# Kernel optimization log

Measured on AMD Instinct MI355X. Metric: run time of the kernel, lower is better.

The kernel has to match this reference:

```python
import jax, jax.numpy as jnp
from jax import lax
import numpy as np

GAMMA = 0.1      # sinkhorn_alpha
EPS = 0.005      # stop_thr
MAXITERS = 1000  # OT_max_iter
TINY = 1e-30


def _pairwise_sq_dist(x, y):
    return (jnp.sum(x * x, axis=1, keepdims=True)
            + jnp.sum(y * y, axis=1)[None, :]
            - 2.0 * (x @ y.T))


def _sinkhorn(M, r, c):
    # M: (B,H,W); r: (1,H); c: (1,W). Faithful to _sinkhorn_inline.
    r_ = r[:, :, None]          # (1,H,1)
    c_ = c[:, None, :]          # (1,W,1 -> 1,1,W)
    M_min = jnp.min(M, axis=2, keepdims=True)
    P0 = jnp.exp(-GAMMA * (M - M_min))

    def cond(state):
        _, err, it = state
        return (err > EPS) & (it < MAXITERS)

    def body(state):
        P, _, it = state
        alpha = jnp.sum(P, axis=2, keepdims=True)
        P1 = P / jnp.maximum(alpha, TINY) * r_
        beta = jnp.sum(P1, axis=1, keepdims=True)
        err = jnp.max(jnp.sum(jnp.abs(beta - c_), axis=2))
        P2 = P1 / jnp.maximum(beta, TINY) * c_
        # torch breaks BEFORE the column update when converged -> keep P1 then
        Pn = jnp.where(err <= EPS, P1, P2)
        return Pn, err, it + 1

    init = (P0, jnp.asarray(jnp.inf, M.dtype), jnp.asarray(0, jnp.int32))
    P, _, _ = lax.while_loop(cond, body, init)
    return P


def setup_inputs() -> dict:
    key = jax.random.key(0)
    k1, k2 = jax.random.split(key)
    x = jax.random.normal(k1, (1024, 512), dtype=jnp.float32)
    y = jax.random.normal(k2, (16384, 512), dtype=jnp.float32)
    return {"x": x, "y": y}


def reference(x, y):
    M = _pairwise_sq_dist(x, y)           # (n, m)
    n, m = M.shape
    # init_a_dist / init_b_dist are None -> uniform marginals (already normalized)
    a = jnp.full((1, n), 1.0 / n, dtype=M.dtype)
    b = jnp.full((1, m), 1.0 / m, dtype=M.dtype)
    # n <= m by construction -> implicit path takes the non-transpose branch
    P = _sinkhorn(M[None], a, b)[0]       # (n, m)
    loss_ETP = jnp.sum(P * M)
    return loss_ETP, P
```

## Files before the change

### kernel.cpp

```cpp
#include <hip/hip_runtime.h>

#define N_ROWS 1024
#define M_COLS 16384
#define DIM 512

constexpr float GAMMA_ = 0.1f;
constexpr float INV_GAMMA = 10.0f;
constexpr float EPS_ = 0.005f;
constexpr float TINY_ = 1e-30f;
constexpr float RVAL = 1.0f / 1024.0f;
constexpr float CVAL = 1.0f / 16384.0f;

typedef __attribute__((ext_vector_type(8))) short bf16x8;
typedef __attribute__((ext_vector_type(4))) float f32x4;

__device__ __forceinline__ float waveRedSum(float v) {
#pragma unroll
    for (int o = 32; o > 0; o >>= 1) v += __shfl_down(v, o);
    return v;
}
__device__ __forceinline__ float waveRedMin(float v) {
#pragma unroll
    for (int o = 32; o > 0; o >>= 1) v = fminf(v, __shfl_down(v, o));
    return v;
}

__device__ __forceinline__ unsigned sysloadu(const unsigned* p) {
    return __hip_atomic_load(p, __ATOMIC_RELAXED, __HIP_MEMORY_SCOPE_SYSTEM);
}
__device__ __forceinline__ void sysstoreu(unsigned* p, unsigned v) {
    __hip_atomic_store(p, v, __ATOMIC_RELAXED, __HIP_MEMORY_SCOPE_SYSTEM);
}
__device__ __forceinline__ float sysloadf(const float* p) {
    return __hip_atomic_load(p, __ATOMIC_RELAXED, __HIP_MEMORY_SCOPE_SYSTEM);
}
__device__ __forceinline__ void sysstoref(float* p, float v) {
    __hip_atomic_store(p, v, __ATOMIC_RELAXED, __HIP_MEMORY_SCOPE_SYSTEM);
}

__device__ __forceinline__ void gbarx(unsigned* __restrict__ arr, unsigned* __restrict__ bcast,
                                      int b, int tid, unsigned e) {
    __syncthreads();
    if (tid == 0) sysstoreu(&arr[b], e);
    if (b == 0) {
        if (tid < 256) {
            while (sysloadu(&arr[tid]) < e) __builtin_amdgcn_s_sleep(1);
        }
        __syncthreads();
        if (tid == 0) sysstoreu(bcast, e);
    } else {
        if (tid == 0) {
            while (sysloadu(bcast) < e) __builtin_amdgcn_s_sleep(1);
        }
    }
    __syncthreads();
}

__device__ __forceinline__ unsigned bf16b(float f) {
    unsigned u = __float_as_uint(f);
    return (u + 0x7FFFu + ((u >> 16) & 1u)) >> 16;
}

__global__ void conv_x(const float* __restrict__ X, unsigned short* __restrict__ xh,
                       unsigned short* __restrict__ xl, float* __restrict__ sx) {
    const int row = blockIdx.x, t = threadIdx.x;
    const float* xr = X + (size_t)row * DIM + t * 8;
    float4 a = *(const float4*)xr, c = *(const float4*)(xr + 4);
    float v[8] = {a.x, a.y, a.z, a.w, c.x, c.y, c.z, c.w};
    unsigned hs[8], ls[8];
    float sq = 0.f;
#pragma unroll
    for (int j = 0; j < 8; ++j) {
        unsigned h = bf16b(v[j]);
        hs[j] = h;
        ls[j] = bf16b(v[j] - __uint_as_float(h << 16));
        sq = fmaf(v[j], v[j], sq);
    }
    uint4 hv = make_uint4(hs[0] | (hs[1] << 16), hs[2] | (hs[3] << 16),
                          hs[4] | (hs[5] << 16), hs[6] | (hs[7] << 16));
    uint4 lv = make_uint4(ls[0] | (ls[1] << 16), ls[2] | (ls[3] << 16),
                          ls[4] | (ls[5] << 16), ls[6] | (ls[7] << 16));
    const size_t off = (size_t)row * 1024 + t * 16;
    *(uint4*)((char*)xh + off) = hv;
    *(uint4*)((char*)xl + off) = lv;
    sq = waveRedSum(sq);
    if (t == 0) sx[row] = sq;
}

__global__ void conv_y(const float* __restrict__ Y, unsigned short* __restrict__ yh,
                       unsigned short* __restrict__ yl, float* __restrict__ sy) {
    const int row = blockIdx.x, t = threadIdx.x;
    const float* yr = Y + (size_t)row * DIM + t * 8;
    float4 a = *(const float4*)yr, c = *(const float4*)(yr + 4);
    float v[8] = {a.x, a.y, a.z, a.w, c.x, c.y, c.z, c.w};
    unsigned hs[8], ls[8];
    float sq = 0.f;
#pragma unroll
    for (int j = 0; j < 8; ++j) {
        unsigned h = bf16b(v[j]);
        hs[j] = h;
        ls[j] = bf16b(v[j] - __uint_as_float(h << 16));
        sq = fmaf(v[j], v[j], sq);
    }
    uint4 hv = make_uint4(hs[0] | (hs[1] << 16), hs[2] | (hs[3] << 16),
                          hs[4] | (hs[5] << 16), hs[6] | (hs[7] << 16));
    uint4 lv = make_uint4(ls[0] | (ls[1] << 16), ls[2] | (ls[3] << 16),
                          ls[4] | (ls[5] << 16), ls[6] | (ls[7] << 16));
    const size_t off = ((size_t)row * 1024 + t * 16) ^ ((size_t)((row & 7) << 4));
    *(uint4*)((char*)yh + off) = hv;
    *(uint4*)((char*)yl + off) = lv;
    sq = waveRedSum(sq);
    if (t == 0) sy[row] = sq;
}

__global__ void init_state(float* __restrict__ ubuf, unsigned* __restrict__ bar,
                           float* __restrict__ out) {
    int idx = blockIdx.x * blockDim.x + threadIdx.x;
    if (idx < 512) bar[idx] = 0u;
    if (idx < 1024) { ubuf[idx] = 1.0f; ubuf[1024 + idx] = 1.0f; }
    if (idx == 0) out[0] = 0.0f;
}

__global__ __launch_bounds__(1024, 4) void sinkhorn_full(
        const unsigned short* __restrict__ xh, const unsigned short* __restrict__ xl,
        const unsigned short* __restrict__ yh, const unsigned short* __restrict__ yl,
        const float* __restrict__ sx, const float* __restrict__ sy,
        float* __restrict__ ubuf, float* __restrict__ Mming,
        float* __restrict__ out, unsigned* __restrict__ bar) {
    const int tid = threadIdx.x;
    const int b = blockIdx.x;
    const int lane = tid & 63;
    const int w = tid >> 6;
    const int l15 = lane & 15;
    const int q = lane >> 4;
    float* Pbuf = out + 1;
    float* spart = out + 4;
    float* errpart = out + 270000;
    unsigned* arr = bar;
    unsigned* bcast = bar + 288;

    __shared__ __align__(16) char ldsY[131072];
    __shared__ float sx_lds[1024];
    __shared__ float mmin_lds[1024];
    __shared__ float u_lds[1024];
    __shared__ float sy_lds[64];
    __shared__ float v_lds[2][64];
    __shared__ float t_acc[16][68];
    __shared__ float red[16];
    __shared__ float sh_err;

    {
        const char* ysrcH = (const char*)yh + (size_t)b * 65536;
        const char* ysrcL = (const char*)yl + (size_t)b * 65536;
#pragma unroll
        for (int p = 0; p < 4; ++p) {
            const int d = tid * 16 + p * 16384;
            *(uint4*)(ldsY + d) = *(const uint4*)(ysrcH + d);
            *(uint4*)(ldsY + 65536 + d) = *(const uint4*)(ysrcL + d);
        }
        sx_lds[tid] = sx[tid];
        if (tid < 64) {
            sy_lds[tid] = sy[(b << 6) + tid];
            v_lds[0][tid] = 1.0f;
            v_lds[1][tid] = 1.0f;
        }
    }
    __syncthreads();

    f32x4 kf[4][4] = {};
    {
        const int rowbase = (w << 6) + l15;
        const int kofs = q * 8;
#pragma unroll 1
        for (int ks = 0; ks < 16; ++ks) {
            bf16x8 ah[4], al[4], bh[4], bl[4];
#pragma unroll
            for (int i = 0; i < 4; ++i) {
                const size_t xo = (size_t)(rowbase + i * 16) * 512 + ks * 32 + kofs;
                ah[i] = *(const bf16x8*)(xh + xo);
                al[i] = *(const bf16x8*)(xl + xo);
                const int cl = i * 16 + l15;
                const int bo = (cl * 1024 + ks * 64 + q * 16) ^ ((cl & 7) << 4);
                bh[i] = *(const bf16x8*)(ldsY + bo);
                bl[i] = *(const bf16x8*)(ldsY + 65536 + bo);
            }
#pragma unroll
            for (int i = 0; i < 4; ++i)
#pragma unroll
                for (int j = 0; j < 4; ++j) {
                    kf[i][j] = __builtin_amdgcn_mfma_f32_16x16x32_bf16(ah[i], bh[j], kf[i][j], 0, 0, 0);
                    kf[i][j] = __builtin_amdgcn_mfma_f32_16x16x32_bf16(ah[i], bl[j], kf[i][j], 0, 0, 0);
                    kf[i][j] = __builtin_amdgcn_mfma_f32_16x16x32_bf16(al[i], bh[j], kf[i][j], 0, 0, 0);
                }
        }
    }
#pragma unroll
    for (int i = 0; i < 4; ++i)
#pragma unroll
        for (int j = 0; j < 4; ++j) {
            const float syv = sy_lds[j * 16 + l15];
#pragma unroll
            for (int reg = 0; reg < 4; ++reg) {
                const int r = (w << 6) + i * 16 + (q << 2) + reg;
                kf[i][j][reg] = sx_lds[r] + syv - 2.0f * kf[i][j][reg];
            }
        }
    {
        float mn[4][4];
#pragma unroll
        for (int i = 0; i < 4; ++i)
#pragma unroll
            for (int reg = 0; reg < 4; ++reg) {
                float m = fminf(fminf(kf[i][0][reg], kf[i][1][reg]),
                                fminf(kf[i][2][reg], kf[i][3][reg]));
#pragma unroll
                for (int o = 1; o < 16; o <<= 1) m = fminf(m, __shfl_xor(m, o));
                mn[i][reg] = m;
            }
        if (l15 == 0) {
#pragma unroll
            for (int i = 0; i < 4; ++i)
#pragma unroll
                for (int reg = 0; reg < 4; ++reg) {
                    const int r = (w << 6) + i * 16 + (q << 2) + reg;
                    sysstoref(&spart[(size_t)r * 256 + b], mn[i][reg]);
                }
        }
    }
    gbarx(arr, bcast, b, tid, 1u);
    if (w >= 1 && w <= 4) {
        const int r = (b << 2) + (w - 1);
        const float* sp = spart + (size_t)r * 256;
        float m = fminf(fminf(sysloadf(&sp[lane]), sysloadf(&sp[lane + 64])),
                        fminf(sysloadf(&sp[lane + 128]), sysloadf(&sp[lane + 192])));
        m = waveRedMin(m);
        if (lane == 0) sysstoref(&Mming[r], m);
    }
    gbarx(arr, bcast, b, tid, 2u);
    if (tid < 256) {
#pragma unroll
        for (int k2 = 0; k2 < 4; ++k2) mmin_lds[tid * 4 + k2] = sysloadf(&Mming[tid * 4 + k2]);
    }
    __syncthreads();
#pragma unroll
    for (int i = 0; i < 4; ++i)
#pragma unroll
        for (int j = 0; j < 4; ++j)
#pragma unroll
            for (int reg = 0; reg < 4; ++reg) {
                const int r = (w << 6) + i * 16 + (q << 2) + reg;
                kf[i][j][reg] = __expf(-GAMMA_ * (kf[i][j][reg] - mmin_lds[r]));
            }

    int cur = 0, vsel = 0, brk = 0;
    unsigned ep = 3u;
    int it = 0;
    for (;; ++it, ep += 2u) {
        {
            float vv[4];
#pragma unroll
            for (int j = 0; j < 4; ++j) vv[j] = v_lds[cur][j * 16 + l15];
            float rs[4][4];
#pragma unroll
            for (int i = 0; i < 4; ++i)
#pragma unroll
                for (int reg = 0; reg < 4; ++reg) {
                    float p = kf[i][0][reg] * vv[0];
                    p = fmaf(kf[i][1][reg], vv[1], p);
                    p = fmaf(kf[i][2][reg], vv[2], p);
                    p = fmaf(kf[i][3][reg], vv[3], p);
#pragma unroll
                    for (int o = 1; o < 16; o <<= 1) p += __shfl_xor(p, o);
                    rs[i][reg] = p;
                }
            if (l15 == 0) {
#pragma unroll
                for (int i = 0; i < 4; ++i)
#pragma unroll
                    for (int reg = 0; reg < 4; ++reg) {
                        const int r = (w << 6) + i * 16 + (q << 2) + reg;
                        sysstoref(&spart[(size_t)r * 256 + b], rs[i][reg]);
                    }
            }
        }
        gbarx(arr, bcast, b, tid, ep);
        float* uOld = ubuf + (((it & 1) ^ 1) << 10);
        float* uNew = ubuf + ((it & 1) << 10);
        {
            if (w == 0) {
                float e = 0.f;
                if (it > 0)
                    e = sysloadf(&errpart[lane]) + sysloadf(&errpart[lane + 64]) +
                        sysloadf(&errpart[lane + 128]) + sysloadf(&errpart[lane + 192]);
                e = waveRedSum(e);
                if (lane == 0) sh_err = (it > 0) ? e : 1e30f;
            } else if (w <= 4) {
                const int r = (b << 2) + (w - 1);
                const float* sp = spart + (size_t)r * 256;
                float s = sysloadf(&sp[lane]) + sysloadf(&sp[lane + 64]) +
                          sysloadf(&sp[lane + 128]) + sysloadf(&sp[lane + 192]);
                s = waveRedSum(s);
                if (lane == 0) {
                    float uo = sysloadf(&uOld[r]);
                    sysstoref(&uNew[r], uo * RVAL / fmaxf(uo * s, TINY_));
                }
            }
        }
        __syncthreads();
        float err = sh_err;
        brk = (err <= EPS_) ? 1 : ((it == 1000) ? 2 : 0);
        gbarx(arr, bcast, b, tid, ep + 1u);
        if (brk) { vsel = (brk == 1) ? (cur ^ 1) : cur; break; }
        if (tid < 256) {
#pragma unroll
            for (int k2 = 0; k2 < 4; ++k2) u_lds[tid * 4 + k2] = sysloadf(&uNew[tid * 4 + k2]);
        }
        __syncthreads();
        {
            float uu[4][4];
#pragma unroll
            for (int i = 0; i < 4; ++i)
#pragma unroll
                for (int reg = 0; reg < 4; ++reg)
                    uu[i][reg] = u_lds[(w << 6) + i * 16 + (q << 2) + reg];
            float tj[4];
#pragma unroll
            for (int j = 0; j < 4; ++j) {
                float t = 0.f;
#pragma unroll
                for (int i = 0; i < 4; ++i)
#pragma unroll
                    for (int reg = 0; reg < 4; ++reg)
                        t = fmaf(kf[i][j][reg], uu[i][reg], t);
                t += __shfl_xor(t, 16);
                t += __shfl_xor(t, 32);
                tj[j] = t;
            }
            if (q == 0) {
#pragma unroll
                for (int j = 0; j < 4; ++j) t_acc[w][j * 16 + l15] = tj[j];
            }
        }
        __syncthreads();
        if (tid < 64) {
            float t = 0.f;
#pragma unroll
            for (int w2 = 0; w2 < 16; ++w2) t += t_acc[w2][tid];
            float vc = v_lds[cur][tid];
            float beta = vc * t;
            float e = fabsf(beta - CVAL);
            v_lds[cur ^ 1][tid] = vc * CVAL / fmaxf(beta, TINY_);
            e = waveRedSum(e);
            if (tid == 0) sysstoref(&errpart[b], e);
        }
        __syncthreads();
        cur ^= 1;
    }

    const float* uEpi = ubuf + (((it & 1) ^ 1) << 10);
    if (tid < 256) {
#pragma unroll
        for (int k2 = 0; k2 < 4; ++k2) u_lds[tid * 4 + k2] = sysloadf(&uEpi[tid * 4 + k2]);
    }
    __syncthreads();
    float vv[4];
#pragma unroll
    for (int j = 0; j < 4; ++j) vv[j] = v_lds[vsel][j * 16 + l15];
    float lsum = 0.f;
#pragma unroll
    for (int i = 0; i < 4; ++i)
#pragma unroll
        for (int reg = 0; reg < 4; ++reg) {
            const int r = (w << 6) + i * 16 + (q << 2) + reg;
            const float ur = u_lds[r];
            const float mmr = mmin_lds[r];
            float* prow = Pbuf + (size_t)r * M_COLS + (b << 6) + l15;
#pragma unroll
            for (int j = 0; j < 4; ++j) {
                float kv = kf[i][j][reg];
                float p = 0.f;
                if (kv > 0.f) {
                    p = ur * kv * vv[j];
                    lsum = fmaf(p, mmr - __logf(kv) * INV_GAMMA, lsum);
                }
                prow[j * 16] = p;
            }
        }
    lsum = waveRedSum(lsum);
    if (lane == 0) red[w] = lsum;
    __syncthreads();
    if (tid == 0) {
        float s = 0.f;
#pragma unroll
        for (int i2 = 0; i2 < 16; ++i2) s += red[i2];
        atomicAdd(out, s);
    }
}

extern "C" void kernel_launch(void* const* d_in, const int* in_sizes, int n_in,
                              void* d_out, int out_size, void* d_ws, size_t ws_size,
                              hipStream_t stream) {
    const float* x = (const float*)d_in[0];
    const float* y = (const float*)d_in[1];
    float* out = (float*)d_out;
    float* ws = (float*)d_ws;
    float* sx   = ws;
    float* sy   = ws + 1024;
    float* Mming = ws + 17408;
    float* ubuf = ws + 18432;
    unsigned* bar = (unsigned*)(ws + 20480);

    unsigned short* xh = (unsigned short*)(out + 300000);
    unsigned short* xl = (unsigned short*)(out + 600000);
    unsigned short* yh = (unsigned short*)(out + 900000);
    unsigned short* yl = (unsigned short*)(out + 5200000);

    conv_x<<<N_ROWS, 64, 0, stream>>>(x, xh, xl, sx);
    conv_y<<<M_COLS, 64, 0, stream>>>(y, yh, yl, sy);
    init_state<<<4, 256, 0, stream>>>(ubuf, bar, out);
    {
        const unsigned short *xhc = xh, *xlc = xl, *yhc = yh, *ylc = yl;
        const float *sxc = sx, *syc = sy;
        void* args[] = {(void*)&xhc, (void*)&xlc, (void*)&yhc, (void*)&ylc,
                        (void*)&sxc, (void*)&syc, (void*)&ubuf, (void*)&Mming,
                        (void*)&out, (void*)&bar};
        hipLaunchCooperativeKernel((const void*)sinkhorn_full, dim3(256), dim3(1024), args, 0, stream);
    }
}
```

Measured before the change: 235.8 us.

## Replace two-barrier-per-iteration grid sync with a hierarchical per-XCD tree exchange

Swaps the centralized global barrier, and the extra reduction phase that followed it, for a two-level tree exchange. Blocks are grouped by XCD (b&7), eight leader blocks reduce their group's partials, and every block then combines the eight group results itself. Every block now computes the full u vector redundantly in LDS instead of going through a global u buffer, and the column error is carried along with the next iteration's row partials. This cuts the global barriers per Sinkhorn iteration from two to one and removes the u broadcast round trip, at the cost of more redundant reads by each block and larger scratch buffers placed far into the output region.

```diff
diff --git a/kernel.cpp b/kernel.cpp
--- a/kernel.cpp
+++ b/kernel.cpp
@@ -19,11 +19,6 @@
     for (int o = 32; o > 0; o >>= 1) v += __shfl_down(v, o);
     return v;
 }
-__device__ __forceinline__ float waveRedMin(float v) {
-#pragma unroll
-    for (int o = 32; o > 0; o >>= 1) v = fminf(v, __shfl_down(v, o));
-    return v;
-}
 
 __device__ __forceinline__ unsigned sysloadu(const unsigned* p) {
     return __hip_atomic_load(p, __ATOMIC_RELAXED, __HIP_MEMORY_SCOPE_SYSTEM);
@@ -36,29 +31,61 @@
 }
 __device__ __forceinline__ void sysstoref(float* p, float v) {
     __hip_atomic_store(p, v, __ATOMIC_RELAXED, __HIP_MEMORY_SCOPE_SYSTEM);
-}
-
-__device__ __forceinline__ void gbarx(unsigned* __restrict__ arr, unsigned* __restrict__ bcast,
-                                      int b, int tid, unsigned e) {
-    __syncthreads();
-    if (tid == 0) sysstoreu(&arr[b], e);
-    if (b == 0) {
-        if (tid < 256) {
-            while (sysloadu(&arr[tid]) < e) __builtin_amdgcn_s_sleep(1);
-        }
-        __syncthreads();
-        if (tid == 0) sysstoreu(bcast, e);
-    } else {
-        if (tid == 0) {
-            while (sysloadu(bcast) < e) __builtin_amdgcn_s_sleep(1);
-        }
-    }
-    __syncthreads();
 }
 
 __device__ __forceinline__ unsigned bf16b(float f) {
     unsigned u = __float_as_uint(f);
     return (u + 0x7FFFu + ((u >> 16) & 1u)) >> 16;
+}
+
+template<bool MINOP>
+__device__ __forceinline__ float tree_exchange(float* __restrict__ spart2,
+        float* __restrict__ sxcd, unsigned* __restrict__ warr,
+        unsigned* __restrict__ xcdrep, const int b, const int tid,
+        const int p, const unsigned ep, const bool doErr) {
+    const int g = b & 7, w32 = b >> 3;
+    __syncthreads();
+    if (tid == 0) sysstoreu(&warr[(g << 5) + w32], ep);
+    if (b < 8) {
+        if (tid < 32) {
+            while (sysloadu(&warr[(b << 5) + tid]) < ep) __builtin_amdgcn_s_sleep(1);
+        }
+        __syncthreads();
+        {
+            const float* sp = spart2 + ((size_t)((p << 3) + b) * 1056 + tid) * 32;
+            float tv[32];
+#pragma unroll
+            for (int i = 0; i < 32; ++i) tv[i] = sysloadf(&sp[i]);
+            float v0 = tv[0];
+#pragma unroll
+            for (int i = 1; i < 32; ++i) v0 = MINOP ? fminf(v0, tv[i]) : (v0 + tv[i]);
+            sysstoref(&sxcd[((size_t)p * 1025 + tid) * 8 + b], v0);
+            if (!MINOP && doErr && tid == 0) {
+                const float* epr = spart2 + ((size_t)((p << 3) + b) * 1056 + 1024) * 32;
+                float ev[32];
+#pragma unroll
+                for (int i = 0; i < 32; ++i) ev[i] = sysloadf(&epr[i]);
+                float es = ev[0];
+#pragma unroll
+                for (int i = 1; i < 32; ++i) es += ev[i];
+                sysstoref(&sxcd[((size_t)p * 1025 + 1024) * 8 + b], es);
+            }
+        }
+        __syncthreads();
+        if (tid < 32) sysstoreu(&xcdrep[(b << 5) + tid], ep);
+    }
+    if (tid < 8) {
+        while (sysloadu(&xcdrep[(tid << 5) + w32]) < ep) __builtin_amdgcn_s_sleep(1);
+    }
+    __syncthreads();
+    const float* sr = sxcd + ((size_t)p * 1025 + tid) * 8;
+    float rv[8];
+#pragma unroll
+    for (int i = 0; i < 8; ++i) rv[i] = sysloadf(&sr[i]);
+    float r = rv[0];
+#pragma unroll
+    for (int i = 1; i < 8; ++i) r = MINOP ? fminf(r, rv[i]) : (r + rv[i]);
+    return r;
 }
 
 __global__ void conv_x(const float* __restrict__ X, unsigned short* __restrict__ xh,
@@ -113,41 +140,40 @@
     if (t == 0) sy[row] = sq;
 }
 
-__global__ void init_state(float* __restrict__ ubuf, unsigned* __restrict__ bar,
-                           float* __restrict__ out) {
+__global__ void init_state(unsigned* __restrict__ flags, float* __restrict__ out) {
     int idx = blockIdx.x * blockDim.x + threadIdx.x;
-    if (idx < 512) bar[idx] = 0u;
-    if (idx < 1024) { ubuf[idx] = 1.0f; ubuf[1024 + idx] = 1.0f; }
+    if (idx < 512) flags[idx] = 0u;
     if (idx == 0) out[0] = 0.0f;
 }
 
-__global__ __launch_bounds__(1024, 4) void sinkhorn_full(
+__global__ __launch_bounds__(1024) void sinkhorn_full(
         const unsigned short* __restrict__ xh, const unsigned short* __restrict__ xl,
         const unsigned short* __restrict__ yh, const unsigned short* __restrict__ yl,
         const float* __restrict__ sx, const float* __restrict__ sy,
-        float* __restrict__ ubuf, float* __restrict__ Mming,
-        float* __restrict__ out, unsigned* __restrict__ bar) {
+        float* __restrict__ sxcd, unsigned* __restrict__ flags,
+        float* __restrict__ out) {
     const int tid = threadIdx.x;
     const int b = blockIdx.x;
     const int lane = tid & 63;
     const int w = tid >> 6;
     const int l15 = lane & 15;
     const int q = lane >> 4;
+    const int g = b & 7, w32 = b >> 3;
     float* Pbuf = out + 1;
-    float* spart = out + 4;
-    float* errpart = out + 270000;
-    unsigned* arr = bar;
-    unsigned* bcast = bar + 288;
+    float* spart2 = out + 10000000;
+    unsigned* warr = flags;
+    unsigned* xcdrep = flags + 256;
 
     __shared__ __align__(16) char ldsY[131072];
     __shared__ float sx_lds[1024];
     __shared__ float mmin_lds[1024];
-    __shared__ float u_lds[1024];
+    __shared__ float u_lds[2][1024];
     __shared__ float sy_lds[64];
     __shared__ float v_lds[2][64];
     __shared__ float t_acc[16][68];
     __shared__ float red[16];
     __shared__ float sh_err;
+    __shared__ float sh_eprev;
 
     {
         const char* ysrcH = (const char*)yh + (size_t)b * 65536;
@@ -159,11 +185,14 @@
             *(uint4*)(ldsY + 65536 + d) = *(const uint4*)(ysrcL + d);
         }
         sx_lds[tid] = sx[tid];
+        u_lds[0][tid] = 1.0f;
+        u_lds[1][tid] = 1.0f;
         if (tid < 64) {
             sy_lds[tid] = sy[(b << 6) + tid];
             v_lds[0][tid] = 1.0f;
             v_lds[1][tid] = 1.0f;
         }
+        if (tid == 0) { sh_eprev = 0.0f; }
     }
     __syncthreads();
 
@@ -223,24 +252,11 @@
 #pragma unroll
                 for (int reg = 0; reg < 4; ++reg) {
                     const int r = (w << 6) + i * 16 + (q << 2) + reg;
-                    sysstoref(&spart[(size_t)r * 256 + b], mn[i][reg]);
+                    sysstoref(&spart2[((size_t)g * 1056 + r) * 32 + w32], mn[i][reg]);
                 }
         }
     }
-    gbarx(arr, bcast, b, tid, 1u);
-    if (w >= 1 && w <= 4) {
-        const int r = (b << 2) + (w - 1);
-        const float* sp = spart + (size_t)r * 256;
-        float m = fminf(fminf(sysloadf(&sp[lane]), sysloadf(&sp[lane + 64])),
-                        fminf(sysloadf(&sp[lane + 128]), sysloadf(&sp[lane + 192])));
-        m = waveRedMin(m);
-        if (lane == 0) sysstoref(&Mming[r], m);
-    }
-    gbarx(arr, bcast, b, tid, 2u);
-    if (tid < 256) {
-#pragma unroll
-        for (int k2 = 0; k2 < 4; ++k2) mmin_lds[tid * 4 + k2] = sysloadf(&Mming[tid * 4 + k2]);
-    }
+    mmin_lds[tid] = tree_exchange<true>(spart2, sxcd, warr, xcdrep, b, tid, 0, 1u, false);
     __syncthreads();
 #pragma unroll
     for (int i = 0; i < 4; ++i)
@@ -253,9 +269,10 @@
             }
 
     int cur = 0, vsel = 0, brk = 0;
-    unsigned ep = 3u;
     int it = 0;
-    for (;; ++it, ep += 2u) {
+    for (;; ++it) {
+        const int p = it & 1;
+        const unsigned ep = (unsigned)it + 2u;
         {
             float vv[4];
 #pragma unroll
@@ -265,13 +282,13 @@
             for (int i = 0; i < 4; ++i)
 #pragma unroll
                 for (int reg = 0; reg < 4; ++reg) {
-                    float p = kf[i][0][reg] * vv[0];
-                    p = fmaf(kf[i][1][reg], vv[1], p);
-                    p = fmaf(kf[i][2][reg], vv[2], p);
-                    p = fmaf(kf[i][3][reg], vv[3], p);
-#pragma unroll
-                    for (int o = 1; o < 16; o <<= 1) p += __shfl_xor(p, o);
-                    rs[i][reg] = p;
+                    float pp = kf[i][0][reg] * vv[0];
+                    pp = fmaf(kf[i][1][reg], vv[1], pp);
+                    pp = fmaf(kf[i][2][reg], vv[2], pp);
+                    pp = fmaf(kf[i][3][reg], vv[3], pp);
+#pragma unroll
+                    for (int o = 1; o < 16; o <<= 1) pp += __shfl_xor(pp, o);
+                    rs[i][reg] = pp;
                 }
             if (l15 == 0) {
 #pragma unroll
@@ -279,50 +296,40 @@
 #pragma unroll
                     for (int reg = 0; reg < 4; ++reg) {
                         const int r = (w << 6) + i * 16 + (q << 2) + reg;
-                        sysstoref(&spart[(size_t)r * 256 + b], rs[i][reg]);
+                        sysstoref(&spart2[((size_t)((p << 3) + g) * 1056 + r) * 32 + w32], rs[i][reg]);
                     }
             }
-        }
-        gbarx(arr, bcast, b, tid, ep);
-        float* uOld = ubuf + (((it & 1) ^ 1) << 10);
-        float* uNew = ubuf + ((it & 1) << 10);
+            if (tid == 0)
+                sysstoref(&spart2[((size_t)((p << 3) + g) * 1056 + 1024) * 32 + w32], sh_eprev);
+        }
+        float srow = tree_exchange<false>(spart2, sxcd, warr, xcdrep, b, tid, p, ep, true);
         {
-            if (w == 0) {
-                float e = 0.f;
-                if (it > 0)
-                    e = sysloadf(&errpart[lane]) + sysloadf(&errpart[lane + 64]) +
-                        sysloadf(&errpart[lane + 128]) + sysloadf(&errpart[lane + 192]);
-                e = waveRedSum(e);
-                if (lane == 0) sh_err = (it > 0) ? e : 1e30f;
-            } else if (w <= 4) {
-                const int r = (b << 2) + (w - 1);
-                const float* sp = spart + (size_t)r * 256;
-                float s = sysloadf(&sp[lane]) + sysloadf(&sp[lane + 64]) +
-                          sysloadf(&sp[lane + 128]) + sysloadf(&sp[lane + 192]);
-                s = waveRedSum(s);
-                if (lane == 0) {
-                    float uo = sysloadf(&uOld[r]);
-                    sysstoref(&uNew[r], uo * RVAL / fmaxf(uo * s, TINY_));
-                }
-            }
+            float uo = u_lds[p ^ 1][tid];
+            u_lds[p][tid] = uo * RVAL / fmaxf(uo * srow, TINY_);
+        }
+        if (tid == 0) {
+            float e = 0.f;
+            if (it > 0) {
+                const float* er = sxcd + ((size_t)p * 1025 + 1024) * 8;
+                float ev[8];
+#pragma unroll
+                for (int i = 0; i < 8; ++i) ev[i] = sysloadf(&er[i]);
+#pragma unroll
+                for (int i = 0; i < 8; ++i) e += ev[i];
+            }
+            sh_err = (it > 0) ? e : 1e30f;
         }
         __syncthreads();
         float err = sh_err;
         brk = (err <= EPS_) ? 1 : ((it == 1000) ? 2 : 0);
-        gbarx(arr, bcast, b, tid, ep + 1u);
         if (brk) { vsel = (brk == 1) ? (cur ^ 1) : cur; break; }
-        if (tid < 256) {
-#pragma unroll
-            for (int k2 = 0; k2 < 4; ++k2) u_lds[tid * 4 + k2] = sysloadf(&uNew[tid * 4 + k2]);
-        }
-        __syncthreads();
         {
             float uu[4][4];
 #pragma unroll
             for (int i = 0; i < 4; ++i)
 #pragma unroll
                 for (int reg = 0; reg < 4; ++reg)
-                    uu[i][reg] = u_lds[(w << 6) + i * 16 + (q << 2) + reg];
+                    uu[i][reg] = u_lds[p][(w << 6) + i * 16 + (q << 2) + reg];
             float tj[4];
 #pragma unroll
             for (int j = 0; j < 4; ++j) {
@@ -351,18 +358,13 @@
             float e = fabsf(beta - CVAL);
             v_lds[cur ^ 1][tid] = vc * CVAL / fmaxf(beta, TINY_);
             e = waveRedSum(e);
-            if (tid == 0) sysstoref(&errpart[b], e);
+            if (tid == 0) sh_eprev = e;
         }
         __syncthreads();
         cur ^= 1;
     }
 
-    const float* uEpi = ubuf + (((it & 1) ^ 1) << 10);
-    if (tid < 256) {
-#pragma unroll
-        for (int k2 = 0; k2 < 4; ++k2) u_lds[tid * 4 + k2] = sysloadf(&uEpi[tid * 4 + k2]);
-    }
-    __syncthreads();
+    const int usel = (it & 1) ^ 1;
     float vv[4];
 #pragma unroll
     for (int j = 0; j < 4; ++j) vv[j] = v_lds[vsel][j * 16 + l15];
@@ -372,18 +374,18 @@
 #pragma unroll
         for (int reg = 0; reg < 4; ++reg) {
             const int r = (w << 6) + i * 16 + (q << 2) + reg;
-            const float ur = u_lds[r];
+            const float ur = u_lds[usel][r];
             const float mmr = mmin_lds[r];
             float* prow = Pbuf + (size_t)r * M_COLS + (b << 6) + l15;
 #pragma unroll
             for (int j = 0; j < 4; ++j) {
                 float kv = kf[i][j][reg];
-                float p = 0.f;
+                float pv = 0.f;
                 if (kv > 0.f) {
-                    p = ur * kv * vv[j];
-                    lsum = fmaf(p, mmr - __logf(kv) * INV_GAMMA, lsum);
+                    pv = ur * kv * vv[j];
+                    lsum = fmaf(pv, mmr - __logf(kv) * INV_GAMMA, lsum);
                 }
-                prow[j * 16] = p;
+                prow[j * 16] = pv;
             }
         }
     lsum = waveRedSum(lsum);
@@ -406,9 +408,8 @@
     float* ws = (float*)d_ws;
     float* sx   = ws;
     float* sy   = ws + 1024;
-    float* Mming = ws + 17408;
-    float* ubuf = ws + 18432;
-    unsigned* bar = (unsigned*)(ws + 20480);
+    float* sxcd = ws + 18432;
+    unsigned* flags = (unsigned*)(ws + 36864);
 
     unsigned short* xh = (unsigned short*)(out + 300000);
     unsigned short* xl = (unsigned short*)(out + 600000);
@@ -417,13 +418,13 @@
 
     conv_x<<<N_ROWS, 64, 0, stream>>>(x, xh, xl, sx);
     conv_y<<<M_COLS, 64, 0, stream>>>(y, yh, yl, sy);
-    init_state<<<4, 256, 0, stream>>>(ubuf, bar, out);
+    init_state<<<2, 256, 0, stream>>>(flags, out);
     {
         const unsigned short *xhc = xh, *xlc = xl, *yhc = yh, *ylc = yl;
         const float *sxc = sx, *syc = sy;
         void* args[] = {(void*)&xhc, (void*)&xlc, (void*)&yhc, (void*)&ylc,
-                        (void*)&sxc, (void*)&syc, (void*)&ubuf, (void*)&Mming,
-                        (void*)&out, (void*)&bar};
+                        (void*)&sxc, (void*)&syc, (void*)&sxcd, (void*)&flags,
+                        (void*)&out};
         hipLaunchCooperativeKernel((const void*)sinkhorn_full, dim3(256), dim3(1024), args, 0, stream);
     }
 }
```

Result: slower. 355.8 us (+50.9%).

## Fuse Y bf16 split into Sinkhorn kernel and coalesce partial-sum exchange

Applied to the files above, without the earlier changes.

Removes the separate conv_y kernel. Each block now loads its 64 Y rows straight from fp32, splits them into bf16 hi/lo parts in LDS and computes the row squared norms locally. The global exchange of per-row partial sums is restructured: each block stages its 1024 values in LDS and writes them contiguously. The per-block error value is also piggybacked into the same buffer, which removes a separate errpart store per iteration. The cost is an extra __syncthreads per iteration and strided cross-block reads on the reduction side.

```diff
diff --git a/kernel.cpp b/kernel.cpp
--- a/kernel.cpp
+++ b/kernel.cpp
@@ -87,46 +87,20 @@
     if (t == 0) sx[row] = sq;
 }
 
-__global__ void conv_y(const float* __restrict__ Y, unsigned short* __restrict__ yh,
-                       unsigned short* __restrict__ yl, float* __restrict__ sy) {
-    const int row = blockIdx.x, t = threadIdx.x;
-    const float* yr = Y + (size_t)row * DIM + t * 8;
-    float4 a = *(const float4*)yr, c = *(const float4*)(yr + 4);
-    float v[8] = {a.x, a.y, a.z, a.w, c.x, c.y, c.z, c.w};
-    unsigned hs[8], ls[8];
-    float sq = 0.f;
-#pragma unroll
-    for (int j = 0; j < 8; ++j) {
-        unsigned h = bf16b(v[j]);
-        hs[j] = h;
-        ls[j] = bf16b(v[j] - __uint_as_float(h << 16));
-        sq = fmaf(v[j], v[j], sq);
-    }
-    uint4 hv = make_uint4(hs[0] | (hs[1] << 16), hs[2] | (hs[3] << 16),
-                          hs[4] | (hs[5] << 16), hs[6] | (hs[7] << 16));
-    uint4 lv = make_uint4(ls[0] | (ls[1] << 16), ls[2] | (ls[3] << 16),
-                          ls[4] | (ls[5] << 16), ls[6] | (ls[7] << 16));
-    const size_t off = ((size_t)row * 1024 + t * 16) ^ ((size_t)((row & 7) << 4));
-    *(uint4*)((char*)yh + off) = hv;
-    *(uint4*)((char*)yl + off) = lv;
-    sq = waveRedSum(sq);
-    if (t == 0) sy[row] = sq;
-}
-
-__global__ void init_state(float* __restrict__ ubuf, unsigned* __restrict__ bar,
+__global__ void init_state(float* __restrict__ ubuf, unsigned* __restrict__ flags,
                            float* __restrict__ out) {
     int idx = blockIdx.x * blockDim.x + threadIdx.x;
-    if (idx < 512) bar[idx] = 0u;
-    if (idx < 1024) { ubuf[idx] = 1.0f; ubuf[1024 + idx] = 1.0f; }
+    if (idx < 512) flags[idx] = 0u;
+    if (idx < 512) { ubuf[idx * 4] = 1.0f; ubuf[idx * 4 + 1] = 1.0f;
+                     ubuf[idx * 4 + 2] = 1.0f; ubuf[idx * 4 + 3] = 1.0f; }
     if (idx == 0) out[0] = 0.0f;
 }
 
 __global__ __launch_bounds__(1024, 4) void sinkhorn_full(
         const unsigned short* __restrict__ xh, const unsigned short* __restrict__ xl,
-        const unsigned short* __restrict__ yh, const unsigned short* __restrict__ yl,
-        const float* __restrict__ sx, const float* __restrict__ sy,
+        const float* __restrict__ Y, const float* __restrict__ sx,
         float* __restrict__ ubuf, float* __restrict__ Mming,
-        float* __restrict__ out, unsigned* __restrict__ bar) {
+        float* __restrict__ out, unsigned* __restrict__ flags) {
     const int tid = threadIdx.x;
     const int b = blockIdx.x;
     const int lane = tid & 63;
@@ -134,10 +108,9 @@
     const int l15 = lane & 15;
     const int q = lane >> 4;
     float* Pbuf = out + 1;
-    float* spart = out + 4;
-    float* errpart = out + 270000;
-    unsigned* arr = bar;
-    unsigned* bcast = bar + 288;
+    float* spart2 = out + 10000000;
+    unsigned* arr = flags;
+    unsigned* bcast = flags + 288;
 
     __shared__ __align__(16) char ldsY[131072];
     __shared__ float sx_lds[1024];
@@ -146,24 +119,48 @@
     __shared__ float sy_lds[64];
     __shared__ float v_lds[2][64];
     __shared__ float t_acc[16][68];
+    __shared__ float srow_lds[16][64];
     __shared__ float red[16];
     __shared__ float sh_err;
+    __shared__ float sh_eprev;
 
     {
-        const char* ysrcH = (const char*)yh + (size_t)b * 65536;
-        const char* ysrcL = (const char*)yl + (size_t)b * 65536;
-#pragma unroll
-        for (int p = 0; p < 4; ++p) {
-            const int d = tid * 16 + p * 16384;
-            *(uint4*)(ldsY + d) = *(const uint4*)(ysrcH + d);
-            *(uint4*)(ldsY + 65536 + d) = *(const uint4*)(ysrcL + d);
-        }
+        const int row = tid >> 4;
+        const int c = tid & 15;
+        const float* yr = Y + (size_t)((b << 6) + row) * DIM + c * 32;
+        const int swz = (row & 7) << 4;
+        float sq = 0.f;
+#pragma unroll
+        for (int s2 = 0; s2 < 4; ++s2) {
+            float4 f0 = *(const float4*)(yr + s2 * 8);
+            float4 f1 = *(const float4*)(yr + s2 * 8 + 4);
+            float v8[8] = {f0.x, f0.y, f0.z, f0.w, f1.x, f1.y, f1.z, f1.w};
+            unsigned h[8], lo[8];
+#pragma unroll
+            for (int j = 0; j < 8; ++j) {
+                h[j] = bf16b(v8[j]);
+                lo[j] = bf16b(v8[j] - __uint_as_float(h[j] << 16));
+                sq = fmaf(v8[j], v8[j], sq);
+            }
+            const int off = (row * 1024 + c * 64 + s2 * 16) ^ swz;
+            *(uint4*)(ldsY + off) = make_uint4(h[0] | (h[1] << 16), h[2] | (h[3] << 16),
+                                               h[4] | (h[5] << 16), h[6] | (h[7] << 16));
+            *(uint4*)(ldsY + 65536 + off) = make_uint4(lo[0] | (lo[1] << 16), lo[2] | (lo[3] << 16),
+                                                       lo[4] | (lo[5] << 16), lo[6] | (lo[7] << 16));
+        }
+        float* sy_part = (float*)t_acc;
+        sy_part[row * 17 + c] = sq;
         sx_lds[tid] = sx[tid];
-        if (tid < 64) {
-            sy_lds[tid] = sy[(b << 6) + tid];
-            v_lds[0][tid] = 1.0f;
-            v_lds[1][tid] = 1.0f;
-        }
+        if (tid < 64) { v_lds[0][tid] = 1.0f; v_lds[1][tid] = 1.0f; }
+        if (tid == 0) sh_eprev = 0.0f;
+    }
+    __syncthreads();
+    if (tid < 64) {
+        const float* sy_part = (const float*)t_acc;
+        float s = 0.f;
+#pragma unroll
+        for (int c2 = 0; c2 < 16; ++c2) s += sy_part[tid * 17 + c2];
+        sy_lds[tid] = s;
     }
     __syncthreads();
 
@@ -221,18 +218,19 @@
 #pragma unroll
             for (int i = 0; i < 4; ++i)
 #pragma unroll
-                for (int reg = 0; reg < 4; ++reg) {
-                    const int r = (w << 6) + i * 16 + (q << 2) + reg;
-                    sysstoref(&spart[(size_t)r * 256 + b], mn[i][reg]);
-                }
-        }
+                for (int reg = 0; reg < 4; ++reg)
+                    srow_lds[w][i * 16 + (q << 2) + reg] = mn[i][reg];
+        }
+        __syncthreads();
+        sysstoref(&spart2[(size_t)b * 1056 + (w << 6) + lane], srow_lds[w][lane]);
     }
     gbarx(arr, bcast, b, tid, 1u);
     if (w >= 1 && w <= 4) {
         const int r = (b << 2) + (w - 1);
-        const float* sp = spart + (size_t)r * 256;
-        float m = fminf(fminf(sysloadf(&sp[lane]), sysloadf(&sp[lane + 64])),
-                        fminf(sysloadf(&sp[lane + 128]), sysloadf(&sp[lane + 192])));
+        float m = fminf(fminf(sysloadf(&spart2[(size_t)lane * 1056 + r]),
+                              sysloadf(&spart2[(size_t)(lane + 64) * 1056 + r])),
+                        fminf(sysloadf(&spart2[(size_t)(lane + 128) * 1056 + r]),
+                              sysloadf(&spart2[(size_t)(lane + 192) * 1056 + r])));
         m = waveRedMin(m);
         if (lane == 0) sysstoref(&Mming[r], m);
     }
@@ -253,9 +251,9 @@
             }
 
     int cur = 0, vsel = 0, brk = 0;
-    unsigned ep = 3u;
     int it = 0;
-    for (;; ++it, ep += 2u) {
+    for (;; ++it) {
+        const unsigned ep = 3u + 2u * (unsigned)it;
         {
             float vv[4];
 #pragma unroll
@@ -265,23 +263,24 @@
             for (int i = 0; i < 4; ++i)
 #pragma unroll
                 for (int reg = 0; reg < 4; ++reg) {
-                    float p = kf[i][0][reg] * vv[0];
-                    p = fmaf(kf[i][1][reg], vv[1], p);
-                    p = fmaf(kf[i][2][reg], vv[2], p);
-                    p = fmaf(kf[i][3][reg], vv[3], p);
-#pragma unroll
-                    for (int o = 1; o < 16; o <<= 1) p += __shfl_xor(p, o);
-                    rs[i][reg] = p;
+                    float pp = kf[i][0][reg] * vv[0];
+                    pp = fmaf(kf[i][1][reg], vv[1], pp);
+                    pp = fmaf(kf[i][2][reg], vv[2], pp);
+                    pp = fmaf(kf[i][3][reg], vv[3], pp);
+#pragma unroll
+                    for (int o = 1; o < 16; o <<= 1) pp += __shfl_xor(pp, o);
+                    rs[i][reg] = pp;
                 }
             if (l15 == 0) {
 #pragma unroll
                 for (int i = 0; i < 4; ++i)
 #pragma unroll
-                    for (int reg = 0; reg < 4; ++reg) {
-                        const int r = (w << 6) + i * 16 + (q << 2) + reg;
-                        sysstoref(&spart[(size_t)r * 256 + b], rs[i][reg]);
-                    }
-            }
+                    for (int reg = 0; reg < 4; ++reg)
+                        srow_lds[w][i * 16 + (q << 2) + reg] = rs[i][reg];
+            }
+            __syncthreads();
+            sysstoref(&spart2[(size_t)b * 1056 + (w << 6) + lane], srow_lds[w][lane]);
+            if (tid == 0) sysstoref(&spart2[(size_t)b * 1056 + 1024], sh_eprev);
         }
         gbarx(arr, bcast, b, tid, ep);
         float* uOld = ubuf + (((it & 1) ^ 1) << 10);
@@ -290,15 +289,18 @@
             if (w == 0) {
                 float e = 0.f;
                 if (it > 0)
-                    e = sysloadf(&errpart[lane]) + sysloadf(&errpart[lane + 64]) +
-                        sysloadf(&errpart[lane + 128]) + sysloadf(&errpart[lane + 192]);
+                    e = sysloadf(&spart2[(size_t)lane * 1056 + 1024]) +
+                        sysloadf(&spart2[(size_t)(lane + 64) * 1056 + 1024]) +
+                        sysloadf(&spart2[(size_t)(lane + 128) * 1056 + 1024]) +
+                        sysloadf(&spart2[(size_t)(lane + 192) * 1056 + 1024]);
                 e = waveRedSum(e);
                 if (lane == 0) sh_err = (it > 0) ? e : 1e30f;
             } else if (w <= 4) {
                 const int r = (b << 2) + (w - 1);
-                const float* sp = spart + (size_t)r * 256;
-                float s = sysloadf(&sp[lane]) + sysloadf(&sp[lane + 64]) +
-                          sysloadf(&sp[lane + 128]) + sysloadf(&sp[lane + 192]);
+                float s = sysloadf(&spart2[(size_t)lane * 1056 + r]) +
+                          sysloadf(&spart2[(size_t)(lane + 64) * 1056 + r]) +
+                          sysloadf(&spart2[(size_t)(lane + 128) * 1056 + r]) +
+                          sysloadf(&spart2[(size_t)(lane + 192) * 1056 + r]);
                 s = waveRedSum(s);
                 if (lane == 0) {
                     float uo = sysloadf(&uOld[r]);
@@ -351,7 +353,7 @@
             float e = fabsf(beta - CVAL);
             v_lds[cur ^ 1][tid] = vc * CVAL / fmaxf(beta, TINY_);
             e = waveRedSum(e);
-            if (tid == 0) sysstoref(&errpart[b], e);
+            if (tid == 0) sh_eprev = e;
         }
         __syncthreads();
         cur ^= 1;
@@ -378,12 +380,12 @@
 #pragma unroll
             for (int j = 0; j < 4; ++j) {
                 float kv = kf[i][j][reg];
-                float p = 0.f;
+                float pv = 0.f;
                 if (kv > 0.f) {
-                    p = ur * kv * vv[j];
-                    lsum = fmaf(p, mmr - __logf(kv) * INV_GAMMA, lsum);
+                    pv = ur * kv * vv[j];
+                    lsum = fmaf(pv, mmr - __logf(kv) * INV_GAMMA, lsum);
                 }
-                prow[j * 16] = p;
+                prow[j * 16] = pv;
             }
         }
     lsum = waveRedSum(lsum);
@@ -404,26 +406,21 @@
     const float* y = (const float*)d_in[1];
     float* out = (float*)d_out;
     float* ws = (float*)d_ws;
-    float* sx   = ws;
-    float* sy   = ws + 1024;
-    float* Mming = ws + 17408;
-    float* ubuf = ws + 18432;
-    unsigned* bar = (unsigned*)(ws + 20480);
+    float* sx    = ws;
+    float* Mming = ws + 1024;
+    float* ubuf  = ws + 2048;
+    unsigned* flags = (unsigned*)(ws + 4096);
 
     unsigned short* xh = (unsigned short*)(out + 300000);
     unsigned short* xl = (unsigned short*)(out + 600000);
-    unsigned short* yh = (unsigned short*)(out + 900000);
-    unsigned short* yl = (unsigned short*)(out + 5200000);
 
     conv_x<<<N_ROWS, 64, 0, stream>>>(x, xh, xl, sx);
-    conv_y<<<M_COLS, 64, 0, stream>>>(y, yh, yl, sy);
-    init_state<<<4, 256, 0, stream>>>(ubuf, bar, out);
+    init_state<<<2, 256, 0, stream>>>(ubuf, flags, out);
     {
-        const unsigned short *xhc = xh, *xlc = xl, *yhc = yh, *ylc = yl;
-        const float *sxc = sx, *syc = sy;
-        void* args[] = {(void*)&xhc, (void*)&xlc, (void*)&yhc, (void*)&ylc,
-                        (void*)&sxc, (void*)&syc, (void*)&ubuf, (void*)&Mming,
-                        (void*)&out, (void*)&bar};
+        const unsigned short *xhc = xh, *xlc = xl;
+        const float *yc = y, *sxc = sx;
+        void* args[] = {(void*)&xhc, (void*)&xlc, (void*)&yc, (void*)&sxc,
+                        (void*)&ubuf, (void*)&Mming, (void*)&out, (void*)&flags};
         hipLaunchCooperativeKernel((const void*)sinkhorn_full, dim3(256), dim3(1024), args, 0, stream);
     }
 }
```

Measured after the change: 208.5 us, median of 2. 11.6% less time.
